# Kernel tuning notes

Measured on AMD Instinct MI355X. Metric: run time of the kernel, lower is better.

## Reference

```python
import jax, jax.numpy as jnp
import numpy as np

N = 200000       # n_nodes
D = 128          # memory_dimension
E = 100000       # number of unique event source nodes this batch
OUTPUT = 30.0    # time-decay constant for embeddings
LAMB = 1.0 * OUTPUT  # self.lamb = lamb * output, used by memory updater
SLOPE = 0.01     # LeakyReLU default negative slope
EPS = 1e-10


def _leaky(x):
    return jnp.where(x >= 0, x, SLOPE * x)


def setup_inputs() -> dict:
    key = jax.random.key(0)
    ks = jax.random.split(key, 10)
    # memory: [N, D+1]; first D cols = exp-weighted message sum, last col = decayed event count (>=1)
    memory = jax.random.uniform(ks[0], (N, D + 1), dtype=jnp.float32)
    memory = memory.at[:, D].add(1.0)
    last_update = jax.random.uniform(ks[1], (N,), dtype=jnp.float32) * 50.0
    # unique sources (aggregator guarantees uniqueness) -> use a random permutation prefix
    unique_sources = jax.random.permutation(ks[2], N)[:E].astype(jnp.int32)
    unique_messages = jax.random.normal(ks[3], (E, D + 1), dtype=jnp.float32) * 0.1
    unique_messages = unique_messages.at[:, D].set(1.0)  # one event per message (ones column)
    # event times after last_update, before now_time
    unique_timestamps = jax.random.uniform(ks[4], (E,), dtype=jnp.float32) * 50.0 + 50.0
    now_time = jnp.float32(110.0)
    static_emb = jax.random.normal(ks[5], (N, D), dtype=jnp.float32) * 0.1
    W1 = jax.random.normal(ks[6], (2 * D, D), dtype=jnp.float32) / np.sqrt(2 * D)
    b1 = jnp.zeros((D,), dtype=jnp.float32)
    W2 = jax.random.normal(ks[7], (D, D), dtype=jnp.float32) / np.sqrt(D)
    b2 = jnp.zeros((D,), dtype=jnp.float32)
    e_lamb = jnp.float32(0.5)
    return {"memory": memory, "last_update": last_update, "unique_messages": unique_messages,
            "unique_timestamps": unique_timestamps, "static_emb": static_emb,
            "W1": W1, "b1": b1, "W2": W2, "b2": b2, "e_lamb": e_lamb,
            "now_time": now_time, "unique_sources": unique_sources}


def reference(memory, last_update, unique_messages, unique_timestamps, static_emb,
              W1, b1, W2, b2, e_lamb, now_time, unique_sources):
    # --- ExpMemoryUpdater.get_updated_memory: exp-decay old state, add new messages, bump last_update
    decay = jnp.exp((last_update[unique_sources] - unique_timestamps) / LAMB)  # [E]
    new_rows = memory[unique_sources] * decay[:, None] + unique_messages       # [E, D+1]
    upd_mem = memory.at[unique_sources].set(new_rows)                          # [N, D+1]
    upd_lu = last_update.at[unique_sources].set(unique_timestamps)             # [N]
    # --- ExpLambsEmbedding over all nodes: [sum/count, sum] -> cat -> [N, 2D]
    msum = upd_mem[:, :D]
    cnt = upd_mem[:, D:D + 1]
    feat = jnp.concatenate([msum / (cnt + EPS), msum], axis=-1)                # [N, 2D]
    # --- embedding_transform: Linear(2D->D) + LeakyReLU + Linear(D->D) + LeakyReLU
    h = _leaky(_leaky(feat @ W1 + b1) @ W2 + b2)                               # [N, D]
    # --- exponential time-decay to 'now'
    dec = h * jnp.exp((upd_lu - now_time) / OUTPUT)[:, None]                   # [N, D]
    # --- learned convex combination with static embedding table
    return e_lamb * static_emb + (1.0 - e_lamb) * dec
```

## Files before the change

kernel.cpp:

```cpp
#include <hip/hip_runtime.h>
#include <hip/hip_bf16.h>

#define N_ROWS 200000
#define DIMS   128
#define E_UPD  100000
#define TILE   64
#define NTILES (N_ROWS / TILE)
#define MSTRIDE 136
#define HSTRIDE 136
#define MAIN_GRID 1024

typedef float f32x4 __attribute__((ext_vector_type(4)));
typedef __bf16 bf16x8 __attribute__((ext_vector_type(8)));
typedef unsigned short u16x8 __attribute__((ext_vector_type(8)));

static __device__ __forceinline__ unsigned short f2b(float f) {
    __hip_bfloat16 b = __float2bfloat16(f);
    return __builtin_bit_cast(unsigned short, b);
}

__global__ void fill_inv(int* inv, int* counter) {
    int i = blockIdx.x * blockDim.x + threadIdx.x;
    if (i < N_ROWS) inv[i] = -1;
    if (i == 0) counter[0] = 0;
}

__global__ void scatter_inv(const int* __restrict__ src, int* __restrict__ inv) {
    int e = blockIdx.x * blockDim.x + threadIdx.x;
    if (e < E_UPD) inv[src[e]] = e;
}

__launch_bounds__(512, 8)
__global__ void ctdg_main(
    const float* __restrict__ memory,
    const float* __restrict__ last_update,
    const float* __restrict__ umsg,
    const float* __restrict__ uts,
    const float* __restrict__ semb,
    const float* __restrict__ W1,
    const float* __restrict__ b1,
    const float* __restrict__ W2,
    const float* __restrict__ b2,
    const float* __restrict__ e_lamb_p,
    const float* __restrict__ now_p,
    const int*   __restrict__ inv,
    int*         __restrict__ counter,
    float*       __restrict__ out)
{
    __shared__ __align__(16) unsigned short msum_s[TILE][MSTRIDE];
    __shared__ __align__(16) unsigned short h1s[TILE][HSTRIDE];
    __shared__ float rcinv[TILE];
    __shared__ float rscale[TILE];
    __shared__ int   s_tile;

    const int tid  = threadIdx.x;
    const int lane = tid & 63;
    const int wave = tid >> 6;
    const int quad = lane >> 4;
    const int l16  = lane & 15;
    const int wn   = wave * 16;

    u16x8 w1a[4];
    u16x8 w1b[4];
    u16x8 w2f[4];
    #pragma unroll
    for (int t = 0; t < 4; ++t) {
        #pragma unroll
        for (int j = 0; j < 8; ++j) {
            const int kr = t*32 + quad*8 + j;
            w1a[t][j] = f2b(W1[kr*128 + wn + l16]);
            w1b[t][j] = f2b(W1[(128 + kr)*128 + wn + l16]);
            w2f[t][j] = f2b(W2[kr*128 + wn + l16]);
        }
    }
    const float b1v   = b1[wn + l16];
    const float b2v   = b2[wn + l16];
    const float el    = e_lamb_p[0];
    const float nowt  = now_p[0];
    const float inv30 = 1.0f / 30.0f;

    const int r = tid >> 3;
    const int s = tid & 7;

    for (;;) {
        if (tid == 0) s_tile = atomicAdd(counter, 1);
        __syncthreads();
        const int tile = s_tile;
        if (tile >= NTILES) break;
        const int row0 = tile * TILE;

        {
            const int g = row0 + r;
            const float lu = last_update[g];
            const int   e  = inv[g];
            const float mc = memory[(size_t)g*129 + 128];
            const float* mrow = memory + (size_t)g*129;
            float d, cnt, lun;
            if (e >= 0) {
                const float ts = uts[e];
                d   = __expf((lu - ts) * inv30);
                cnt = fmaf(mc, d, umsg[(size_t)e*129 + 128]);
                lun = ts;
            } else {
                d = 1.0f; cnt = mc; lun = lu;
            }
            if (s == 0) {
                rcinv[r]  = 1.0f / (cnt + 1e-10f);
                rscale[r] = __expf((lun - nowt) * inv30);
            }
            if (e >= 0) {
                const float* grow = umsg + (size_t)e*129;
                #pragma unroll
                for (int j = 0; j < 8; ++j) {
                    const int c = 2*s + 16*j;
                    const float m0 = fmaf(mrow[c],   d, grow[c]);
                    const float m1 = fmaf(mrow[c+1], d, grow[c+1]);
                    const unsigned pk = (unsigned)f2b(m0) | ((unsigned)f2b(m1) << 16);
                    *(unsigned*)&msum_s[r][c] = pk;
                }
            } else {
                #pragma unroll
                for (int j = 0; j < 8; ++j) {
                    const int c = 2*s + 16*j;
                    const unsigned pk = (unsigned)f2b(mrow[c]) | ((unsigned)f2b(mrow[c+1]) << 16);
                    *(unsigned*)&msum_s[r][c] = pk;
                }
            }
        }
        __syncthreads();

        #pragma unroll
        for (int mt = 0; mt < 4; ++mt) {
            f32x4 aP = {0.f, 0.f, 0.f, 0.f};
            f32x4 aQ = {0.f, 0.f, 0.f, 0.f};
            const int mrow = mt*16 + l16;
            #pragma unroll
            for (int k = 0; k < 4; ++k) {
                u16x8 a = *(const u16x8*)&msum_s[mrow][k*32 + quad*8];
                aP = __builtin_amdgcn_mfma_f32_16x16x32_bf16(
                        __builtin_bit_cast(bf16x8, a),
                        __builtin_bit_cast(bf16x8, w1a[k]), aP, 0, 0, 0);
                aQ = __builtin_amdgcn_mfma_f32_16x16x32_bf16(
                        __builtin_bit_cast(bf16x8, a),
                        __builtin_bit_cast(bf16x8, w1b[k]), aQ, 0, 0, 0);
            }
            #pragma unroll
            for (int rr = 0; rr < 4; ++rr) {
                const int row = mt*16 + quad*4 + rr;
                float v = fmaf(rcinv[row], aP[rr], aQ[rr]) + b1v;
                v = (v >= 0.f) ? v : 0.01f * v;
                h1s[row][wn + l16] = f2b(v);
            }
        }
        __syncthreads();

        #pragma unroll
        for (int mt = 0; mt < 4; ++mt) {
            f32x4 acc = {0.f, 0.f, 0.f, 0.f};
            const int mrow = mt*16 + l16;
            #pragma unroll
            for (int k = 0; k < 4; ++k) {
                u16x8 a = *(const u16x8*)&h1s[mrow][k*32 + quad*8];
                acc = __builtin_amdgcn_mfma_f32_16x16x32_bf16(
                        __builtin_bit_cast(bf16x8, a),
                        __builtin_bit_cast(bf16x8, w2f[k]), acc, 0, 0, 0);
            }
            #pragma unroll
            for (int rr = 0; rr < 4; ++rr) {
                const int row = mt*16 + quad*4 + rr;
                const int g = row0 + row;
                float v = acc[rr] + b2v;
                v = (v >= 0.f) ? v : 0.01f * v;
                v *= rscale[row];
                const float sv = semb[(size_t)g*128 + wn + l16];
                const float o  = el * sv + (1.0f - el) * v;
                __builtin_nontemporal_store(o, &out[(size_t)g*128 + wn + l16]);
            }
        }
        __syncthreads();
    }
}

extern "C" void kernel_launch(void* const* d_in, const int* in_sizes, int n_in,
                              void* d_out, int out_size, void* d_ws, size_t ws_size,
                              hipStream_t stream) {
    const float* memory      = (const float*)d_in[0];
    const float* last_update = (const float*)d_in[1];
    const float* umsg        = (const float*)d_in[2];
    const float* uts         = (const float*)d_in[3];
    const float* semb        = (const float*)d_in[4];
    const float* W1          = (const float*)d_in[5];
    const float* b1          = (const float*)d_in[6];
    const float* W2          = (const float*)d_in[7];
    const float* b2          = (const float*)d_in[8];
    const float* e_lamb      = (const float*)d_in[9];
    const float* nowt        = (const float*)d_in[10];
    const int*   src         = (const int*)d_in[11];

    int* inv     = (int*)d_ws;
    int* counter = inv + N_ROWS;
    float* out   = (float*)d_out;

    fill_inv<<<(N_ROWS + 255) / 256, 256, 0, stream>>>(inv, counter);
    scatter_inv<<<(E_UPD + 255) / 256, 256, 0, stream>>>(src, inv);
    ctdg_main<<<MAIN_GRID, 512, 0, stream>>>(memory, last_update, umsg, uts, semb,
                                             W1, b1, W2, b2, e_lamb, nowt,
                                             inv, counter, out);
}
```

Measured before the change: 387.8 us.

## Prefetch next tile's memory rows into registers and drop trailing barrier

Software-pipelines the persistent tile loop. The next tile index is fetched with the atomic early, and that tile's inv entry and memory row values are loaded into registers during the second GEMM of the current tile. This hides global load latency, and double-buffering rscale and the tile index lets the end-of-iteration barrier be removed. It also lowers the occupancy hint to 6 and the grid to 768 to give room for the extra registers, and switches the output store from nontemporal to a normal store. Running fewer resident waves may reduce latency hiding in other parts of the loop.

```diff
diff --git a/kernel.cpp b/kernel.cpp
--- a/kernel.cpp
+++ b/kernel.cpp
@@ -8,7 +8,7 @@
 #define NTILES (N_ROWS / TILE)
 #define MSTRIDE 136
 #define HSTRIDE 136
-#define MAIN_GRID 1024
+#define MAIN_GRID 768
 
 typedef float f32x4 __attribute__((ext_vector_type(4)));
 typedef __bf16 bf16x8 __attribute__((ext_vector_type(8)));
@@ -30,7 +30,7 @@
     if (e < E_UPD) inv[src[e]] = e;
 }
 
-__launch_bounds__(512, 8)
+__launch_bounds__(512, 6)
 __global__ void ctdg_main(
     const float* __restrict__ memory,
     const float* __restrict__ last_update,
@@ -50,8 +50,8 @@
     __shared__ __align__(16) unsigned short msum_s[TILE][MSTRIDE];
     __shared__ __align__(16) unsigned short h1s[TILE][HSTRIDE];
     __shared__ float rcinv[TILE];
-    __shared__ float rscale[TILE];
-    __shared__ int   s_tile;
+    __shared__ float rscale[2][TILE];
+    __shared__ int   s_next[2];
 
     const int tid  = threadIdx.x;
     const int lane = tid & 63;
@@ -82,19 +82,36 @@
     const int r = tid >> 3;
     const int s = tid & 7;
 
-    for (;;) {
-        if (tid == 0) s_tile = atomicAdd(counter, 1);
-        __syncthreads();
-        const int tile = s_tile;
-        if (tile >= NTILES) break;
+    if (tid == 0) s_next[0] = atomicAdd(counter, 1);
+    __syncthreads();
+    int tile = s_next[0];
+
+    float pm0[8], pm1[8];
+    int   pe = -1;
+    if (tile < NTILES) {
+        const int g = tile*TILE + r;
+        pe = inv[g];
+        const float* mrow = memory + (size_t)g*129;
+        #pragma unroll
+        for (int j = 0; j < 8; ++j) {
+            const int c = 2*s + 16*j;
+            pm0[j] = mrow[c];
+            pm1[j] = mrow[c+1];
+        }
+    }
+
+    int it = 0;
+    while (tile < NTILES) {
         const int row0 = tile * TILE;
-
+        const int par  = it & 1;
+        const int nxt  = par ^ 1;
+
+        if (tid == 0) s_next[nxt] = atomicAdd(counter, 1);
         {
-            const int g = row0 + r;
+            const int g  = row0 + r;
+            const int e  = pe;
             const float lu = last_update[g];
-            const int   e  = inv[g];
             const float mc = memory[(size_t)g*129 + 128];
-            const float* mrow = memory + (size_t)g*129;
             float d, cnt, lun;
             if (e >= 0) {
                 const float ts = uts[e];
@@ -105,30 +122,29 @@
                 d = 1.0f; cnt = mc; lun = lu;
             }
             if (s == 0) {
-                rcinv[r]  = 1.0f / (cnt + 1e-10f);
-                rscale[r] = __expf((lun - nowt) * inv30);
+                rcinv[r]       = 1.0f / (cnt + 1e-10f);
+                rscale[par][r] = __expf((lun - nowt) * inv30);
             }
             if (e >= 0) {
                 const float* grow = umsg + (size_t)e*129;
                 #pragma unroll
                 for (int j = 0; j < 8; ++j) {
                     const int c = 2*s + 16*j;
-                    const float m0 = fmaf(mrow[c],   d, grow[c]);
-                    const float m1 = fmaf(mrow[c+1], d, grow[c+1]);
-                    const unsigned pk = (unsigned)f2b(m0) | ((unsigned)f2b(m1) << 16);
-                    *(unsigned*)&msum_s[r][c] = pk;
+                    const float m0 = fmaf(pm0[j], d, grow[c]);
+                    const float m1 = fmaf(pm1[j], d, grow[c+1]);
+                    *(unsigned*)&msum_s[r][c] = (unsigned)f2b(m0) | ((unsigned)f2b(m1) << 16);
                 }
             } else {
                 #pragma unroll
                 for (int j = 0; j < 8; ++j) {
                     const int c = 2*s + 16*j;
-                    const unsigned pk = (unsigned)f2b(mrow[c]) | ((unsigned)f2b(mrow[c+1]) << 16);
-                    *(unsigned*)&msum_s[r][c] = pk;
+                    *(unsigned*)&msum_s[r][c] = (unsigned)f2b(pm0[j]) | ((unsigned)f2b(pm1[j]) << 16);
                 }
             }
         }
         __syncthreads();
 
+        const int tn = s_next[nxt];
         #pragma unroll
         for (int mt = 0; mt < 4; ++mt) {
             f32x4 aP = {0.f, 0.f, 0.f, 0.f};
@@ -154,6 +170,17 @@
         }
         __syncthreads();
 
+        if (tn < NTILES) {
+            const int g2 = tn*TILE + r;
+            pe = inv[g2];
+            const float* mrow2 = memory + (size_t)g2*129;
+            #pragma unroll
+            for (int j = 0; j < 8; ++j) {
+                const int c = 2*s + 16*j;
+                pm0[j] = mrow2[c];
+                pm1[j] = mrow2[c+1];
+            }
+        }
         #pragma unroll
         for (int mt = 0; mt < 4; ++mt) {
             f32x4 acc = {0.f, 0.f, 0.f, 0.f};
@@ -171,13 +198,13 @@
                 const int g = row0 + row;
                 float v = acc[rr] + b2v;
                 v = (v >= 0.f) ? v : 0.01f * v;
-                v *= rscale[row];
+                v *= rscale[par][row];
                 const float sv = semb[(size_t)g*128 + wn + l16];
-                const float o  = el * sv + (1.0f - el) * v;
-                __builtin_nontemporal_store(o, &out[(size_t)g*128 + wn + l16]);
-            }
-        }
-        __syncthreads();
+                out[(size_t)g*128 + wn + l16] = el * sv + (1.0f - el) * v;
+            }
+        }
+        tile = tn;
+        ++it;
     }
 }
 
```

After: 402.6 us. +3.8%, slower.
